# Kernel optimization log

Hardware: AMD Instinct MI355X
Metric: run time of the kernel (lower is better)

## Reference

```python
import jax, jax.numpy as jnp
import numpy as np
from jax import lax

H = 2048          # hidden_size
I = 1408          # moe_intermediate_size
E = 16            # n_routed_experts
K = 4             # num_experts_per_tok
N_SHARED = 2      # n_shared_experts
IS = I * N_SHARED # shared expert intermediate
B, S = 1, 1024


def setup_inputs() -> dict:
    key = jax.random.key(0)
    ks = jax.random.split(key, 8)
    scale = 0.02
    return {
        "hidden_states": jax.random.normal(ks[0], (B, S, H), dtype=jnp.float32),
        "gate_w": jax.random.normal(ks[1], (E, H), dtype=jnp.float32) * scale,  # MoEGate.weight
        "w_gate": jax.random.normal(ks[2], (E, H, I), dtype=jnp.float32) * scale,
        "w_up": jax.random.normal(ks[3], (E, H, I), dtype=jnp.float32) * scale,
        "w_down": jax.random.normal(ks[4], (E, I, H), dtype=jnp.float32) * scale,
        "sw_gate": jax.random.normal(ks[5], (H, IS), dtype=jnp.float32) * scale,
        "sw_up": jax.random.normal(ks[6], (H, IS), dtype=jnp.float32) * scale,
        "sw_down": jax.random.normal(ks[7], (IS, H), dtype=jnp.float32) * scale,
    }


def _moe_forward(hidden_states, gate_w, w_gate, w_up, w_down, sw_gate, sw_up, sw_down):
    bsz, seq_len, h = hidden_states.shape
    flat = hidden_states.reshape(-1, h)                # [T, H]
    T = flat.shape[0]

    # --- MoEGate: softmax scoring + top-k (norm_topk_prob=False) ---
    logits = flat @ gate_w.T                           # [T, E]
    scores = jax.nn.softmax(logits, axis=-1)
    topk_w, topk_idx = lax.top_k(scores, K)            # [T, K]

    # combine[t, e] = sum of top-k weights assigned to expert e (scatter of dispatch)
    combine = jnp.zeros((T, E), dtype=flat.dtype).at[
        jnp.arange(T)[:, None], topk_idx
    ].add(topk_w)                                      # [T, E]

    # --- routed experts: scan over experts, accumulate weighted SwiGLU MLP outputs ---
    def step(y, xs):
        wg, wu, wd, c = xs                             # [H,I], [H,I], [I,H], [T]
        out = (jax.nn.silu(flat @ wg) * (flat @ wu)) @ wd   # [T, H]
        return y + c[:, None] * out, None

    y, _ = lax.scan(step, jnp.zeros_like(flat), (w_gate, w_up, w_down, combine.T))

    # --- shared experts (always-on SwiGLU MLP with larger intermediate) ---
    shared = (jax.nn.silu(flat @ sw_gate) * (flat @ sw_up)) @ sw_down  # [T, H]

    return (y + shared).reshape(bsz, seq_len, h)


def reference(hidden_states, gate_w, w_gate, w_up, w_down, sw_gate, sw_up, sw_down):
    return _moe_forward(hidden_states, gate_w, w_gate, w_up, w_down,
                        sw_gate, sw_up, sw_down)
```

## Files before the change

### kernel.cpp

```cpp
#include <hip/hip_runtime.h>
#include <hip/hip_bf16.h>
#include <stdint.h>

#define T_TOK 1024
#define H_DIM 2048
#define I_DIM 1408
#define E_NUM 16
#define K_TOP 4
#define IS_DIM 2816
#define BK 64
#define BKP 72
#define BM 128
#define NT_MAX 64

typedef __hip_bfloat16 bf;
typedef __attribute__((ext_vector_type(8))) __bf16 bf16x8;
typedef __attribute__((ext_vector_type(4))) float f32x4;

__device__ __forceinline__ void gload16(const void* g, void* l) {
  __builtin_amdgcn_global_load_lds((const __attribute__((address_space(1))) void*)g,
                                   (__attribute__((address_space(3))) void*)l, 16, 0, 0);
}

__global__ void cvt_x_kernel(const float* __restrict__ in, bf* __restrict__ out) {
  int i = blockIdx.x * blockDim.x + threadIdx.x;
  float4 v = reinterpret_cast<const float4*>(in)[i];
  int b = i * 4;
  out[b + 0] = __float2bfloat16(v.x);
  out[b + 1] = __float2bfloat16(v.y);
  out[b + 2] = __float2bfloat16(v.z);
  out[b + 3] = __float2bfloat16(v.w);
}

__global__ void gate_topk_kernel(const float* __restrict__ x, const float* __restrict__ gw,
                                 int* __restrict__ topk_idx, float* __restrict__ topk_w) {
  int t = blockIdx.x;
  int lane = threadIdx.x;
  float acc[E_NUM];
#pragma unroll
  for (int e = 0; e < E_NUM; e++) acc[e] = 0.f;
  const float* xt = x + (long)t * H_DIM;
  for (int h = lane; h < H_DIM; h += 64) {
    float xv = xt[h];
#pragma unroll
    for (int e = 0; e < E_NUM; e++) acc[e] += xv * gw[e * H_DIM + h];
  }
#pragma unroll
  for (int e = 0; e < E_NUM; e++) {
    float v = acc[e];
    for (int off = 32; off; off >>= 1) v += __shfl_xor(v, off, 64);
    acc[e] = v;
  }
  if (lane == 0) {
    float m = acc[0];
#pragma unroll
    for (int e = 1; e < E_NUM; e++) m = fmaxf(m, acc[e]);
    float sc[E_NUM];
    float s = 0.f;
#pragma unroll
    for (int e = 0; e < E_NUM; e++) { sc[e] = expf(acc[e] - m); s += sc[e]; }
    float inv = 1.f / s;
#pragma unroll
    for (int e = 0; e < E_NUM; e++) sc[e] *= inv;
    for (int k = 0; k < K_TOP; k++) {
      int bi = 0;
      float bv = sc[0];
      for (int e = 1; e < E_NUM; e++)
        if (sc[e] > bv) { bv = sc[e]; bi = e; }
      topk_idx[t * K_TOP + k] = bi;
      topk_w[t * K_TOP + k] = bv;
      sc[bi] = -1.f;
    }
  }
}

__global__ void build_lists_kernel(const int* __restrict__ topk_idx,
                                   int* __restrict__ rows, int* __restrict__ tile_expert,
                                   int* __restrict__ n_tiles) {
  __shared__ int cnt[E_NUM], cur[E_NUM], s_tb;
  int tid = threadIdx.x;
  if (tid < E_NUM) cnt[tid] = 0;
  __syncthreads();
  for (int p = tid; p < T_TOK * K_TOP; p += blockDim.x)
    atomicAdd(&cnt[topk_idx[p]], 1);
  __syncthreads();
  if (tid == 0) {
    int tb = 0;
    for (int e = 0; e < E_NUM; e++) {
      int nt = (cnt[e] + BM - 1) / BM;
      cur[e] = tb * BM;
      for (int j = 0; j < nt; j++) tile_expert[tb + j] = e;
      tb += nt;
    }
    for (int j = 0; j < 16; j++) tile_expert[tb + j] = 16 + (j >> 3);
    s_tb = tb;
    *n_tiles = tb + 16;
  }
  __syncthreads();
  int tb = s_tb;
  for (int r = tid; r < NT_MAX * BM; r += blockDim.x) rows[r] = -1;
  __syncthreads();
  for (int p = tid; p < T_TOK * K_TOP; p += blockDim.x) {
    int t = p >> 2, k = p & 3;
    int e = topk_idx[p];
    int slot = atomicAdd(&cur[e], 1);
    rows[slot] = t * 8 + k;
  }
  for (int idx = tid; idx < 16 * BM; idx += blockDim.x) {
    int j = idx >> 7, r = idx & 127;
    int t = (j & 7) * BM + r;
    rows[(tb + j) * BM + r] = t * 8 + 4 + (j >> 3);
  }
}

__launch_bounds__(256, 2)
__global__ void gemm_gateup_kernel(const bf* __restrict__ xb,
                                   const int* __restrict__ rows,
                                   const int* __restrict__ tile_expert,
                                   const int* __restrict__ n_tiles,
                                   const float* __restrict__ Wg,
                                   const float* __restrict__ Wu,
                                   const float* __restrict__ SWg,
                                   const float* __restrict__ SWu,
                                   bf* __restrict__ act) {
  int bid = blockIdx.x;
  int idx = (bid & 7) * 176 + (bid >> 3);
  int x = idx >> 6, rt = idx & 63;
  if (rt >= *n_tiles) return;
  int e = tile_expert[rt];
  bool sh = e >= 16;
  const float* gbase = sh ? (SWg + (e - 16) * I_DIM) : (Wg + (long)e * H_DIM * I_DIM);
  const float* ubase = sh ? (SWu + (e - 16) * I_DIM) : (Wu + (long)e * H_DIM * I_DIM);
  long bstride = sh ? IS_DIM : I_DIM;
  int i0 = x * 64;

  __shared__ bf lA[2][BM * BK];
  __shared__ bf lB2[2][2][64 * BKP];

  int tid = threadIdx.x, w = tid >> 6, lane = tid & 63;
  int l15 = lane & 15, lhi = lane >> 4;
  int nq = tid & 15, mt = (tid >> 4) & 1, kg = tid >> 5;
  int sswz = (((lane & 7) ^ (lane >> 3)) * 8);
  int bco = (kg ^ (nq & 7)) * 8;

  const bf* asrc[4];
#pragma unroll
  for (int i = 0; i < 4; i++) {
    int rr = rt * BM + i * 32 + w * 8 + (lane >> 3);
    int p = rows[rr];
    int tok = (p >= 0) ? (p >> 3) : 0;
    asrc[i] = xb + (long)tok * H_DIM + sswz;
  }

  const float* psrc = (mt ? ubase : gbase) + i0 + nq * 4 + (long)(kg * 8) * bstride;

  f32x4 accg[4][2], accu[4][2];
  f32x4 z4 = {0.f, 0.f, 0.f, 0.f};
#pragma unroll
  for (int m = 0; m < 4; m++)
#pragma unroll
    for (int n = 0; n < 2; n++) { accg[m][n] = z4; accu[m][n] = z4; }

  int wr = w >> 1, wc = w & 1;
  float4 v[8];

#define GU_ISSUE(T, NB)                                                            \
  {                                                                                \
    const float* p_ = psrc + (long)(T) * BK * bstride;                             \
    _Pragma("unroll") for (int j = 0; j < 8; j++)                                  \
        v[j] = *reinterpret_cast<const float4*>(p_ + (long)j * bstride);           \
    _Pragma("unroll") for (int i = 0; i < 4; i++)                                  \
        gload16(asrc[i] + (T) * BK, &lA[NB][(i * 32 + w * 8) * BK]);               \
  }

#define GU_WRITE(NB)                                                               \
  {                                                                                \
    _Pragma("unroll") for (int c = 0; c < 4; c++) {                                \
      union { bf16x8 vv; bf s[8]; } o;                                             \
      _Pragma("unroll") for (int j = 0; j < 8; j++)                                \
          o.s[j] = __float2bfloat16(((const float*)&v[j])[c]);                     \
      *reinterpret_cast<bf16x8*>(&lB2[NB][mt][(nq * 4 + c) * BKP + bco]) = o.vv;   \
    }                                                                              \
  }

#define GU_MFMA(CB)                                                                \
  {                                                                                \
    _Pragma("unroll") for (int kk = 0; kk < 2; kk++) {                             \
      bf16x8 af[4];                                                                \
      _Pragma("unroll") for (int m = 0; m < 4; m++)                                \
          af[m] = *reinterpret_cast<const bf16x8*>(                                \
              &lA[CB][(wr * 64 + m * 16 + l15) * BK + (((kk * 4 + lhi) ^ (l15 & 7)) * 8)]); \
      _Pragma("unroll") for (int n = 0; n < 2; n++) {                              \
        int nrow = wc * 32 + n * 16 + l15;                                         \
        int bch = ((kk * 4 + lhi) ^ ((nrow >> 2) & 7)) * 8;                        \
        bf16x8 gf = *reinterpret_cast<const bf16x8*>(&lB2[CB][0][nrow * BKP + bch]); \
        bf16x8 uf = *reinterpret_cast<const bf16x8*>(&lB2[CB][1][nrow * BKP + bch]); \
        _Pragma("unroll") for (int m = 0; m < 4; m++) {                            \
          accg[m][n] = __builtin_amdgcn_mfma_f32_16x16x32_bf16(af[m], gf, accg[m][n], 0, 0, 0); \
          accu[m][n] = __builtin_amdgcn_mfma_f32_16x16x32_bf16(af[m], uf, accu[m][n], 0, 0, 0); \
        }                                                                          \
      }                                                                            \
    }                                                                              \
  }

  const int NT = H_DIM / BK;
  GU_ISSUE(0, 0);
  GU_WRITE(0);
  __syncthreads();

  for (int t = 0; t < NT; t += 2) {
    GU_ISSUE(t + 1, 1);
    __builtin_amdgcn_sched_barrier(0);
    GU_MFMA(0);
    __builtin_amdgcn_sched_barrier(0);
    GU_WRITE(1);
    __syncthreads();
    if (t + 2 < NT) GU_ISSUE(t + 2, 0);
    __builtin_amdgcn_sched_barrier(0);
    GU_MFMA(1);
    __builtin_amdgcn_sched_barrier(0);
    if (t + 2 < NT) GU_WRITE(0);
    __syncthreads();
  }
#undef GU_ISSUE
#undef GU_WRITE
#undef GU_MFMA

#pragma unroll
  for (int m = 0; m < 4; m++)
#pragma unroll
    for (int n = 0; n < 2; n++)
#pragma unroll
      for (int r2 = 0; r2 < 4; r2++) {
        float gv = accg[m][n][r2];
        float uv = accu[m][n][r2];
        float s = (gv / (1.f + __expf(-gv))) * uv;
        int row = rt * BM + wr * 64 + m * 16 + lhi * 4 + r2;
        int col = i0 + wc * 32 + n * 16 + l15;
        act[(long)row * I_DIM + col] = __float2bfloat16(s);
      }
}

__launch_bounds__(256, 2)
__global__ void gemm_down_kernel(const bf* __restrict__ A,
                                 const int* __restrict__ rows,
                                 const int* __restrict__ tile_expert,
                                 const int* __restrict__ n_tiles,
                                 const float* __restrict__ Wd,
                                 const float* __restrict__ SWd,
                                 bf* __restrict__ outp) {
  int bid = blockIdx.x;
  int idx = (bid & 7) * 128 + (bid >> 3);
  int x = idx >> 6, rt = idx & 63;
  if (rt >= *n_tiles) return;
  int e = tile_expert[rt];
  bool sh = e >= 16;
  const float* bbase = sh ? (SWd + (long)(e - 16) * I_DIM * H_DIM)
                          : (Wd + (long)e * I_DIM * H_DIM);
  int h0 = x * 128;

  __shared__ bf lA[2][BM * BK];
  __shared__ bf lB[2][128 * BKP];
  __shared__ int rowsl[BM];

  int tid = threadIdx.x, w = tid >> 6, lane = tid & 63;
  int l15 = lane & 15, lhi = lane >> 4;
  int kg = tid >> 5, ng = tid & 31;
  int sswz = (((lane & 7) ^ (lane >> 3)) * 8);
  int bco = (kg ^ (ng & 7)) * 8;
  if (tid < BM) rowsl[tid] = rows[rt * BM + tid];

  const bf* asrc[4];
#pragma unroll
  for (int i = 0; i < 4; i++)
    asrc[i] = A + (long)(rt * BM + i * 32 + w * 8 + (lane >> 3)) * I_DIM + sswz;

  const float* psrc = bbase + h0 + ng * 4 + (long)(kg * 8) * H_DIM;

  f32x4 acc[4][4];
  f32x4 z4 = {0.f, 0.f, 0.f, 0.f};
#pragma unroll
  for (int m = 0; m < 4; m++)
#pragma unroll
    for (int n = 0; n < 4; n++) acc[m][n] = z4;

  int wr = w >> 1, wc = w & 1;
  float4 v[8];

#define DN_ISSUE(T, NB)                                                            \
  {                                                                                \
    const float* p_ = psrc + (long)(T) * BK * H_DIM;                               \
    _Pragma("unroll") for (int j = 0; j < 8; j++)                                  \
        v[j] = *reinterpret_cast<const float4*>(p_ + (long)j * H_DIM);             \
    _Pragma("unroll") for (int i = 0; i < 4; i++)                                  \
        gload16(asrc[i] + (T) * BK, &lA[NB][(i * 32 + w * 8) * BK]);               \
  }

#define DN_WRITE(NB)                                                               \
  {                                                                                \
    _Pragma("unroll") for (int c = 0; c < 4; c++) {                                \
      union { bf16x8 vv; bf s[8]; } o;                                             \
      _Pragma("unroll") for (int j = 0; j < 8; j++)                                \
          o.s[j] = __float2bfloat16(((const float*)&v[j])[c]);                     \
      *reinterpret_cast<bf16x8*>(&lB[NB][(ng * 4 + c) * BKP + bco]) = o.vv;        \
    }                                                                              \
  }

#define DN_MFMA(CB)                                                                \
  {                                                                                \
    _Pragma("unroll") for (int kk = 0; kk < 2; kk++) {                             \
      bf16x8 af[4];                                                                \
      _Pragma("unroll") for (int m = 0; m < 4; m++)                                \
          af[m] = *reinterpret_cast<const bf16x8*>(                                \
              &lA[CB][(wr * 64 + m * 16 + l15) * BK + (((kk * 4 + lhi) ^ (l15 & 7)) * 8)]); \
      _Pragma("unroll") for (int n = 0; n < 4; n++) {                              \
        int nrow = wc * 64 + n * 16 + l15;                                         \
        int bch = ((kk * 4 + lhi) ^ ((nrow >> 2) & 7)) * 8;                        \
        bf16x8 bfr = *reinterpret_cast<const bf16x8*>(&lB[CB][nrow * BKP + bch]);  \
        _Pragma("unroll") for (int m = 0; m < 4; m++)                              \
            acc[m][n] = __builtin_amdgcn_mfma_f32_16x16x32_bf16(af[m], bfr, acc[m][n], 0, 0, 0); \
      }                                                                            \
    }                                                                              \
  }

  const int NT = I_DIM / BK;
  DN_ISSUE(0, 0);
  DN_WRITE(0);
  __syncthreads();

  for (int t = 0; t < NT; t += 2) {
    DN_ISSUE(t + 1, 1);
    __builtin_amdgcn_sched_barrier(0);
    DN_MFMA(0);
    __builtin_amdgcn_sched_barrier(0);
    DN_WRITE(1);
    __syncthreads();
    if (t + 2 < NT) DN_ISSUE(t + 2, 0);
    __builtin_amdgcn_sched_barrier(0);
    DN_MFMA(1);
    __builtin_amdgcn_sched_barrier(0);
    if (t + 2 < NT) DN_WRITE(0);
    __syncthreads();
  }
#undef DN_ISSUE
#undef DN_WRITE
#undef DN_MFMA

#pragma unroll
  for (int m = 0; m < 4; m++)
#pragma unroll
    for (int n = 0; n < 4; n++)
#pragma unroll
      for (int r2 = 0; r2 < 4; r2++) {
        int lrow = wr * 64 + m * 16 + lhi * 4 + r2;
        int col = h0 + wc * 64 + n * 16 + l15;
        int p = rowsl[lrow];
        if (p >= 0) outp[(long)p * H_DIM + col] = __float2bfloat16(acc[m][n][r2]);
      }
}

__global__ void combine_kernel(const bf* __restrict__ outp,
                               const float* __restrict__ topk_w,
                               float* __restrict__ out) {
  int idx = blockIdx.x * blockDim.x + threadIdx.x;
  int t = idx >> 11;
  int h = idx & 2047;
  const bf* base = outp + (long)t * 8 * H_DIM + h;
  float acc = __bfloat162float(base[4 * H_DIM]) + __bfloat162float(base[5 * H_DIM]);
#pragma unroll
  for (int k = 0; k < 4; k++)
    acc += topk_w[t * 4 + k] * __bfloat162float(base[(long)k * H_DIM]);
  out[idx] = acc;
}

extern "C" void kernel_launch(void* const* d_in, const int* in_sizes, int n_in,
                              void* d_out, int out_size, void* d_ws, size_t ws_size,
                              hipStream_t stream) {
  const float* x     = (const float*)d_in[0];
  const float* gw    = (const float*)d_in[1];
  const float* wgate = (const float*)d_in[2];
  const float* wup   = (const float*)d_in[3];
  const float* wdown = (const float*)d_in[4];
  const float* swg   = (const float*)d_in[5];
  const float* swu   = (const float*)d_in[6];
  const float* swd   = (const float*)d_in[7];
  float* out = (float*)d_out;

  char* ws = (char*)d_ws;
  size_t off = 0;
  auto alloc = [&](size_t bytes) {
    void* p = ws + off;
    off += (bytes + 255) & ~(size_t)255;
    return p;
  };

  bf* xb   = (bf*)alloc((size_t)T_TOK * H_DIM * 2);
  bf* act  = (bf*)alloc((size_t)NT_MAX * BM * I_DIM * 2);
  bf* outp = (bf*)alloc((size_t)T_TOK * 8 * H_DIM * 2);
  int*   topk_idx = (int*)alloc(T_TOK * K_TOP * 4);
  float* topk_w   = (float*)alloc(T_TOK * K_TOP * 4);
  int*   rowsbuf  = (int*)alloc(NT_MAX * BM * 4);
  int*   tile_exp = (int*)alloc(NT_MAX * 4);
  int*   n_tiles  = (int*)alloc(64);
  (void)ws_size; (void)in_sizes; (void)n_in; (void)out_size;

  hipLaunchKernelGGL(cvt_x_kernel, dim3(T_TOK * H_DIM / 1024), dim3(256), 0, stream, x, xb);
  hipLaunchKernelGGL(gate_topk_kernel, dim3(T_TOK), dim3(64), 0, stream, x, gw, topk_idx, topk_w);
  hipLaunchKernelGGL(build_lists_kernel, dim3(1), dim3(256), 0, stream, topk_idx, rowsbuf, tile_exp, n_tiles);

  hipLaunchKernelGGL(gemm_gateup_kernel, dim3((I_DIM / 64) * NT_MAX), dim3(256), 0, stream,
                     xb, rowsbuf, tile_exp, n_tiles, wgate, wup, swg, swu, act);
  hipLaunchKernelGGL(gemm_down_kernel, dim3((H_DIM / 128) * NT_MAX), dim3(256), 0, stream,
                     act, rowsbuf, tile_exp, n_tiles, wdown, swd, outp);

  hipLaunchKernelGGL(combine_kernel, dim3(T_TOK * H_DIM / 256), dim3(256), 0, stream,
                     outp, topk_w, out);
}
```

Before: 317.8 us.

## Enlarge MoE GEMM tiles to 256x128 with 512 threads and single-barrier pipeline

New measurement: 333.3 us. 4.9% more time.

```diff
diff --git a/kernel.cpp b/kernel.cpp
--- a/kernel.cpp
+++ b/kernel.cpp
@@ -10,8 +10,9 @@
 #define IS_DIM 2816
 #define BK 64
 #define BKP 72
-#define BM 128
-#define NT_MAX 64
+#define BM 256
+#define BNW 128
+#define NT_MAX 40
 
 typedef __hip_bfloat16 bf;
 typedef __attribute__((ext_vector_type(8))) __bf16 bf16x8;
@@ -92,9 +93,9 @@
       for (int j = 0; j < nt; j++) tile_expert[tb + j] = e;
       tb += nt;
     }
-    for (int j = 0; j < 16; j++) tile_expert[tb + j] = 16 + (j >> 3);
+    for (int j = 0; j < 8; j++) tile_expert[tb + j] = 16 + (j >> 2);
     s_tb = tb;
-    *n_tiles = tb + 16;
+    *n_tiles = tb + 8;
   }
   __syncthreads();
   int tb = s_tb;
@@ -106,14 +107,14 @@
     int slot = atomicAdd(&cur[e], 1);
     rows[slot] = t * 8 + k;
   }
-  for (int idx = tid; idx < 16 * BM; idx += blockDim.x) {
-    int j = idx >> 7, r = idx & 127;
-    int t = (j & 7) * BM + r;
-    rows[(tb + j) * BM + r] = t * 8 + 4 + (j >> 3);
-  }
-}
-
-__launch_bounds__(256, 2)
+  for (int idx = tid; idx < 8 * BM; idx += blockDim.x) {
+    int j = idx >> 8, r = idx & 255;
+    int t = (j & 3) * BM + r;
+    rows[(tb + j) * BM + r] = t * 8 + 4 + (j >> 2);
+  }
+}
+
+__launch_bounds__(512, 2)
 __global__ void gemm_gateup_kernel(const bf* __restrict__ xb,
                                    const int* __restrict__ rows,
                                    const int* __restrict__ tile_expert,
@@ -124,56 +125,58 @@
                                    const float* __restrict__ SWu,
                                    bf* __restrict__ act) {
   int bid = blockIdx.x;
-  int idx = (bid & 7) * 176 + (bid >> 3);
-  int x = idx >> 6, rt = idx & 63;
+  int idx = (bid & 7) * 55 + (bid >> 3);
+  int x = idx / NT_MAX, rt = idx % NT_MAX;
   if (rt >= *n_tiles) return;
   int e = tile_expert[rt];
   bool sh = e >= 16;
   const float* gbase = sh ? (SWg + (e - 16) * I_DIM) : (Wg + (long)e * H_DIM * I_DIM);
   const float* ubase = sh ? (SWu + (e - 16) * I_DIM) : (Wu + (long)e * H_DIM * I_DIM);
   long bstride = sh ? IS_DIM : I_DIM;
-  int i0 = x * 64;
+  int i0 = x * BNW;
 
   __shared__ bf lA[2][BM * BK];
-  __shared__ bf lB2[2][2][64 * BKP];
+  __shared__ bf lB2[2][2][BNW * BKP];
 
   int tid = threadIdx.x, w = tid >> 6, lane = tid & 63;
   int l15 = lane & 15, lhi = lane >> 4;
-  int nq = tid & 15, mt = (tid >> 4) & 1, kg = tid >> 5;
+  int nq = tid & 31, kq = (tid >> 5) & 7, mt = tid >> 8;
   int sswz = (((lane & 7) ^ (lane >> 3)) * 8);
-  int bco = (kg ^ (nq & 7)) * 8;
+  int bco = (kq ^ (nq & 7)) * 8;
 
   const bf* asrc[4];
 #pragma unroll
   for (int i = 0; i < 4; i++) {
-    int rr = rt * BM + i * 32 + w * 8 + (lane >> 3);
+    int rr = rt * BM + i * 64 + w * 8 + (lane >> 3);
     int p = rows[rr];
     int tok = (p >= 0) ? (p >> 3) : 0;
     asrc[i] = xb + (long)tok * H_DIM + sswz;
   }
 
-  const float* psrc = (mt ? ubase : gbase) + i0 + nq * 4 + (long)(kg * 8) * bstride;
-
-  f32x4 accg[4][2], accu[4][2];
+  const float* psrc = (mt ? ubase : gbase) + i0 + nq * 4 + (long)(kq * 8) * bstride;
+
+  f32x4 accg[4][4], accu[4][4];
   f32x4 z4 = {0.f, 0.f, 0.f, 0.f};
 #pragma unroll
   for (int m = 0; m < 4; m++)
 #pragma unroll
-    for (int n = 0; n < 2; n++) { accg[m][n] = z4; accu[m][n] = z4; }
+    for (int n = 0; n < 4; n++) { accg[m][n] = z4; accu[m][n] = z4; }
 
   int wr = w >> 1, wc = w & 1;
   float4 v[8];
 
-#define GU_ISSUE(T, NB)                                                            \
+#define GU_LOADB(T)                                                                \
   {                                                                                \
     const float* p_ = psrc + (long)(T) * BK * bstride;                             \
     _Pragma("unroll") for (int j = 0; j < 8; j++)                                  \
         v[j] = *reinterpret_cast<const float4*>(p_ + (long)j * bstride);           \
+  }
+#define GU_LOADA(T, NB)                                                            \
+  {                                                                                \
     _Pragma("unroll") for (int i = 0; i < 4; i++)                                  \
-        gload16(asrc[i] + (T) * BK, &lA[NB][(i * 32 + w * 8) * BK]);               \
-  }
-
-#define GU_WRITE(NB)                                                               \
+        gload16(asrc[i] + (T) * BK, &lA[NB][(i * 64 + w * 8) * BK]);               \
+  }
+#define GU_WRITEB(NB)                                                              \
   {                                                                                \
     _Pragma("unroll") for (int c = 0; c < 4; c++) {                                \
       union { bf16x8 vv; bf s[8]; } o;                                             \
@@ -182,7 +185,6 @@
       *reinterpret_cast<bf16x8*>(&lB2[NB][mt][(nq * 4 + c) * BKP + bco]) = o.vv;   \
     }                                                                              \
   }
-
 #define GU_MFMA(CB)                                                                \
   {                                                                                \
     _Pragma("unroll") for (int kk = 0; kk < 2; kk++) {                             \
@@ -190,8 +192,8 @@
       _Pragma("unroll") for (int m = 0; m < 4; m++)                                \
           af[m] = *reinterpret_cast<const bf16x8*>(                                \
               &lA[CB][(wr * 64 + m * 16 + l15) * BK + (((kk * 4 + lhi) ^ (l15 & 7)) * 8)]); \
-      _Pragma("unroll") for (int n = 0; n < 2; n++) {                              \
-        int nrow = wc * 32 + n * 16 + l15;                                         \
+      _Pragma("unroll") for (int n = 0; n < 4; n++) {                              \
+        int nrow = wc * 64 + n * 16 + l15;                                         \
         int bch = ((kk * 4 + lhi) ^ ((nrow >> 2) & 7)) * 8;                        \
         bf16x8 gf = *reinterpret_cast<const bf16x8*>(&lB2[CB][0][nrow * BKP + bch]); \
         bf16x8 uf = *reinterpret_cast<const bf16x8*>(&lB2[CB][1][nrow * BKP + bch]); \
@@ -204,44 +206,52 @@
   }
 
   const int NT = H_DIM / BK;
-  GU_ISSUE(0, 0);
-  GU_WRITE(0);
-  __syncthreads();
-
-  for (int t = 0; t < NT; t += 2) {
-    GU_ISSUE(t + 1, 1);
+  GU_LOADB(0);
+  GU_LOADA(0, 0);
+  GU_WRITEB(0);
+  GU_LOADB(1);
+  asm volatile("s_waitcnt vmcnt(8)" ::: "memory");
+  asm volatile("s_waitcnt lgkmcnt(0)" ::: "memory");
+  __builtin_amdgcn_s_barrier();
+  __builtin_amdgcn_sched_barrier(0);
+
+  for (int t = 0; t < NT - 1; ++t) {
+    int cur = t & 1, nxt = cur ^ 1;
+    GU_LOADA(t + 1, nxt);
+    GU_MFMA(cur);
+    GU_WRITEB(nxt);
+    if (t + 2 < NT) {
+      GU_LOADB(t + 2);
+      asm volatile("s_waitcnt vmcnt(8)" ::: "memory");
+    } else {
+      asm volatile("s_waitcnt vmcnt(0)" ::: "memory");
+    }
+    asm volatile("s_waitcnt lgkmcnt(0)" ::: "memory");
+    __builtin_amdgcn_s_barrier();
     __builtin_amdgcn_sched_barrier(0);
-    GU_MFMA(0);
-    __builtin_amdgcn_sched_barrier(0);
-    GU_WRITE(1);
-    __syncthreads();
-    if (t + 2 < NT) GU_ISSUE(t + 2, 0);
-    __builtin_amdgcn_sched_barrier(0);
-    GU_MFMA(1);
-    __builtin_amdgcn_sched_barrier(0);
-    if (t + 2 < NT) GU_WRITE(0);
-    __syncthreads();
-  }
-#undef GU_ISSUE
-#undef GU_WRITE
+  }
+  GU_MFMA((NT - 1) & 1);
+#undef GU_LOADB
+#undef GU_LOADA
+#undef GU_WRITEB
 #undef GU_MFMA
 
 #pragma unroll
   for (int m = 0; m < 4; m++)
 #pragma unroll
-    for (int n = 0; n < 2; n++)
+    for (int n = 0; n < 4; n++)
 #pragma unroll
       for (int r2 = 0; r2 < 4; r2++) {
         float gv = accg[m][n][r2];
         float uv = accu[m][n][r2];
         float s = (gv / (1.f + __expf(-gv))) * uv;
         int row = rt * BM + wr * 64 + m * 16 + lhi * 4 + r2;
-        int col = i0 + wc * 32 + n * 16 + l15;
+        int col = i0 + wc * 64 + n * 16 + l15;
         act[(long)row * I_DIM + col] = __float2bfloat16(s);
       }
 }
 
-__launch_bounds__(256, 2)
+__launch_bounds__(512, 2)
 __global__ void gemm_down_kernel(const bf* __restrict__ A,
                                  const int* __restrict__ rows,
                                  const int* __restrict__ tile_expert,
@@ -250,22 +260,23 @@
                                  const float* __restrict__ SWd,
                                  bf* __restrict__ outp) {
   int bid = blockIdx.x;
-  int idx = (bid & 7) * 128 + (bid >> 3);
-  int x = idx >> 6, rt = idx & 63;
+  int idx = (bid & 7) * 80 + (bid >> 3);
+  int x = idx / NT_MAX, rt = idx % NT_MAX;
   if (rt >= *n_tiles) return;
   int e = tile_expert[rt];
   bool sh = e >= 16;
   const float* bbase = sh ? (SWd + (long)(e - 16) * I_DIM * H_DIM)
                           : (Wd + (long)e * I_DIM * H_DIM);
-  int h0 = x * 128;
+  int h0 = x * BNW;
 
   __shared__ bf lA[2][BM * BK];
-  __shared__ bf lB[2][128 * BKP];
+  __shared__ bf lB[2][BNW * BKP];
   __shared__ int rowsl[BM];
 
   int tid = threadIdx.x, w = tid >> 6, lane = tid & 63;
   int l15 = lane & 15, lhi = lane >> 4;
-  int kg = tid >> 5, ng = tid & 31;
+  int ng = tid & 31, kg = (tid >> 5) & 7;
+  bool stager = tid < 256;
   int sswz = (((lane & 7) ^ (lane >> 3)) * 8);
   int bco = (kg ^ (ng & 7)) * 8;
   if (tid < BM) rowsl[tid] = rows[rt * BM + tid];
@@ -273,7 +284,7 @@
   const bf* asrc[4];
 #pragma unroll
   for (int i = 0; i < 4; i++)
-    asrc[i] = A + (long)(rt * BM + i * 32 + w * 8 + (lane >> 3)) * I_DIM + sswz;
+    asrc[i] = A + (long)(rt * BM + i * 64 + w * 8 + (lane >> 3)) * I_DIM + sswz;
 
   const float* psrc = bbase + h0 + ng * 4 + (long)(kg * 8) * H_DIM;
 
@@ -287,16 +298,18 @@
   int wr = w >> 1, wc = w & 1;
   float4 v[8];
 
-#define DN_ISSUE(T, NB)                                                            \
+#define DN_LOADB(T)                                                                \
   {                                                                                \
     const float* p_ = psrc + (long)(T) * BK * H_DIM;                               \
     _Pragma("unroll") for (int j = 0; j < 8; j++)                                  \
         v[j] = *reinterpret_cast<const float4*>(p_ + (long)j * H_DIM);             \
+  }
+#define DN_LOADA(T, NB)                                                            \
+  {                                                                                \
     _Pragma("unroll") for (int i = 0; i < 4; i++)                                  \
-        gload16(asrc[i] + (T) * BK, &lA[NB][(i * 32 + w * 8) * BK]);               \
-  }
-
-#define DN_WRITE(NB)                                                               \
+        gload16(asrc[i] + (T) * BK, &lA[NB][(i * 64 + w * 8) * BK]);               \
+  }
+#define DN_WRITEB(NB)                                                              \
   {                                                                                \
     _Pragma("unroll") for (int c = 0; c < 4; c++) {                                \
       union { bf16x8 vv; bf s[8]; } o;                                             \
@@ -305,7 +318,6 @@
       *reinterpret_cast<bf16x8*>(&lB[NB][(ng * 4 + c) * BKP + bco]) = o.vv;        \
     }                                                                              \
   }
-
 #define DN_MFMA(CB)                                                                \
   {                                                                                \
     _Pragma("unroll") for (int kk = 0; kk < 2; kk++) {                             \
@@ -324,26 +336,42 @@
   }
 
   const int NT = I_DIM / BK;
-  DN_ISSUE(0, 0);
-  DN_WRITE(0);
-  __syncthreads();
-
-  for (int t = 0; t < NT; t += 2) {
-    DN_ISSUE(t + 1, 1);
+  if (stager) { DN_LOADB(0); }
+  DN_LOADA(0, 0);
+  if (stager) {
+    DN_WRITEB(0);
+    DN_LOADB(1);
+    asm volatile("s_waitcnt vmcnt(8)" ::: "memory");
+  } else {
+    asm volatile("s_waitcnt vmcnt(0)" ::: "memory");
+  }
+  asm volatile("s_waitcnt lgkmcnt(0)" ::: "memory");
+  __builtin_amdgcn_s_barrier();
+  __builtin_amdgcn_sched_barrier(0);
+
+  for (int t = 0; t < NT - 1; ++t) {
+    int cur = t & 1, nxt = cur ^ 1;
+    DN_LOADA(t + 1, nxt);
+    DN_MFMA(cur);
+    if (stager) {
+      DN_WRITEB(nxt);
+      if (t + 2 < NT) {
+        DN_LOADB(t + 2);
+        asm volatile("s_waitcnt vmcnt(8)" ::: "memory");
+      } else {
+        asm volatile("s_waitcnt vmcnt(0)" ::: "memory");
+      }
+    } else {
+      asm volatile("s_waitcnt vmcnt(0)" ::: "memory");
+    }
+    asm volatile("s_waitcnt lgkmcnt(0)" ::: "memory");
+    __builtin_amdgcn_s_barrier();
     __builtin_amdgcn_sched_barrier(0);
-    DN_MFMA(0);
-    __builtin_amdgcn_sched_barrier(0);
-    DN_WRITE(1);
-    __syncthreads();
-    if (t + 2 < NT) DN_ISSUE(t + 2, 0);
-    __builtin_amdgcn_sched_barrier(0);
-    DN_MFMA(1);
-    __builtin_amdgcn_sched_barrier(0);
-    if (t + 2 < NT) DN_WRITE(0);
-    __syncthreads();
-  }
-#undef DN_ISSUE
-#undef DN_WRITE
+  }
+  DN_MFMA((NT - 1) & 1);
+#undef DN_LOADB
+#undef DN_LOADA
+#undef DN_WRITEB
 #undef DN_MFMA
 
 #pragma unroll
@@ -362,15 +390,28 @@
 __global__ void combine_kernel(const bf* __restrict__ outp,
                                const float* __restrict__ topk_w,
                                float* __restrict__ out) {
-  int idx = blockIdx.x * blockDim.x + threadIdx.x;
-  int t = idx >> 11;
-  int h = idx & 2047;
+  int g = blockIdx.x * blockDim.x + threadIdx.x;
+  int t = g >> 8;
+  int h = (g & 255) * 8;
   const bf* base = outp + (long)t * 8 * H_DIM + h;
-  float acc = __bfloat162float(base[4 * H_DIM]) + __bfloat162float(base[5 * H_DIM]);
-#pragma unroll
-  for (int k = 0; k < 4; k++)
-    acc += topk_w[t * 4 + k] * __bfloat162float(base[(long)k * H_DIM]);
-  out[idx] = acc;
+  float w0 = topk_w[t * 4 + 0], w1 = topk_w[t * 4 + 1];
+  float w2 = topk_w[t * 4 + 2], w3 = topk_w[t * 4 + 3];
+  bf16x8 s4 = *reinterpret_cast<const bf16x8*>(base + 4 * H_DIM);
+  bf16x8 s5 = *reinterpret_cast<const bf16x8*>(base + 5 * H_DIM);
+  bf16x8 r0 = *reinterpret_cast<const bf16x8*>(base + 0 * H_DIM);
+  bf16x8 r1 = *reinterpret_cast<const bf16x8*>(base + 1 * H_DIM);
+  bf16x8 r2 = *reinterpret_cast<const bf16x8*>(base + 2 * H_DIM);
+  bf16x8 r3 = *reinterpret_cast<const bf16x8*>(base + 3 * H_DIM);
+  float acc[8];
+#pragma unroll
+  for (int j = 0; j < 8; j++) {
+    acc[j] = (float)s4[j] + (float)s5[j]
+           + w0 * (float)r0[j] + w1 * (float)r1[j]
+           + w2 * (float)r2[j] + w3 * (float)r3[j];
+  }
+  float4* o = reinterpret_cast<float4*>(out + (long)t * H_DIM + h);
+  o[0] = make_float4(acc[0], acc[1], acc[2], acc[3]);
+  o[1] = make_float4(acc[4], acc[5], acc[6], acc[7]);
 }
 
 extern "C" void kernel_launch(void* const* d_in, const int* in_sizes, int n_in,
@@ -408,11 +449,11 @@
   hipLaunchKernelGGL(gate_topk_kernel, dim3(T_TOK), dim3(64), 0, stream, x, gw, topk_idx, topk_w);
   hipLaunchKernelGGL(build_lists_kernel, dim3(1), dim3(256), 0, stream, topk_idx, rowsbuf, tile_exp, n_tiles);
 
-  hipLaunchKernelGGL(gemm_gateup_kernel, dim3((I_DIM / 64) * NT_MAX), dim3(256), 0, stream,
+  hipLaunchKernelGGL(gemm_gateup_kernel, dim3((I_DIM / BNW) * NT_MAX), dim3(512), 0, stream,
                      xb, rowsbuf, tile_exp, n_tiles, wgate, wup, swg, swu, act);
-  hipLaunchKernelGGL(gemm_down_kernel, dim3((H_DIM / 128) * NT_MAX), dim3(256), 0, stream,
+  hipLaunchKernelGGL(gemm_down_kernel, dim3((H_DIM / BNW) * NT_MAX), dim3(512), 0, stream,
                      act, rowsbuf, tile_exp, n_tiles, wdown, swd, outp);
 
-  hipLaunchKernelGGL(combine_kernel, dim3(T_TOK * H_DIM / 256), dim3(256), 0, stream,
+  hipLaunchKernelGGL(combine_kernel, dim3(T_TOK * H_DIM / 8 / 256), dim3(256), 0, stream,
                      outp, topk_w, out);
 }
```
